# Performance work log

Measured on AMD Instinct MI355X. Metric: run time of the kernel, lower is better.

## Reference

```python
import jax, jax.numpy as jnp
import numpy as np

N, E, ENC, EMB, PI = 100000, 1600000, 128, 128, 98
ALPHA1, ALPHA2 = 0.5, 0.5


def setup_inputs() -> dict:
    key = jax.random.key(0)
    ks = jax.random.split(key, 20)
    s = 0.05
    return {
        "x": jax.random.normal(ks[0], (N, ENC), jnp.float32),
        "d2an": jax.random.normal(ks[1], (N, PI), jnp.float32),
        "ei0": jax.random.randint(ks[2], (2, E), 0, N, jnp.int32),
        "ew0": jax.random.uniform(ks[3], (E,), jnp.float32, 0.1, 4.0),
        "ei1": jax.random.randint(ks[4], (2, E), 0, N, jnp.int32),
        "ew1": jax.random.uniform(ks[5], (E,), jnp.float32, 0.1, 4.0),
        "nodeW1": jax.random.normal(ks[6], (ENC, ENC + PI), jnp.float32) * s,
        "nodeW2": jax.random.normal(ks[7], (ENC, ENC + PI), jnp.float32) * s,
        "W1a": jax.random.normal(ks[8], (EMB, ENC), jnp.float32) * s,
        "W1b": jax.random.normal(ks[9], (EMB, ENC), jnp.float32) * s,
        "W2a": jax.random.normal(ks[10], (EMB, ENC), jnp.float32) * s,
        "W2b": jax.random.normal(ks[11], (EMB, ENC), jnp.float32) * s,
        "W3a": jax.random.normal(ks[12], (EMB, EMB), jnp.float32) * s,
        "W3b": jax.random.normal(ks[13], (EMB, EMB), jnp.float32) * s,
        "W4a": jax.random.normal(ks[14], (EMB, EMB), jnp.float32) * s,
        "W4b": jax.random.normal(ks[15], (EMB, EMB), jnp.float32) * s,
    }


def _layer(x, ei, ew, W1, W2, nodeW, d2an, first):
    """PosKnnGNNLayer.forward: add self loops, optional nodeLin, GCN deg norm +
    edge norm, gather -> lin1/lin2 -> scale -> scatter-add (aggr='add')."""
    n = x.shape[0]
    loop = jnp.arange(n, dtype=ei.dtype)
    row = jnp.concatenate([ei[0], loop])          # source nodes (x_j)
    col = jnp.concatenate([ei[1], loop])          # target nodes (aggregation)
    attr = jnp.concatenate([ew, jnp.ones((n,), ew.dtype)])  # self-loop fill=1.0
    if first:
        x = jnp.concatenate([x, d2an], axis=1) @ nodeW.T
    deg = jax.ops.segment_sum(jnp.ones_like(attr), col, num_segments=n)
    dis = jnp.where(deg > 0, jax.lax.rsqrt(jnp.maximum(deg, 1.0)), 0.0)
    deg_norm = dis[row] * dis[col]                # [E']
    einv = attr ** -0.5
    einv = jnp.where(jnp.isinf(einv), 0.0, einv)
    einv = jnp.minimum(einv, 1.0)                 # clamp >1 to 1
    h1 = x @ W1.T                                 # [N, out]
    h2 = x @ W2.T
    msg = deg_norm[:, None] * h1[row] + einv[:, None] * h2[row]  # [E', out]
    return jax.ops.segment_sum(msg, col, num_segments=n)


def reference(x, d2an, ei0, ew0, ei1, ew1, nodeW1, nodeW2,
              W1a, W1b, W2a, W2b, W3a, W3b, W4a, W4b):
    # eval mode: dropout(p=0.3) is identity
    x0 = jax.nn.relu(_layer(x, ei0, ew0, W1a, W1b, nodeW1, d2an, True))
    x1 = jax.nn.relu(_layer(x, ei1, ew1, W2a, W2b, nodeW2, d2an, True))
    xm = ALPHA1 * x0 + ALPHA2 * x1
    x0 = jax.nn.relu(_layer(xm, ei0, ew0, W3a, W3b, None, None, False))
    x1 = jax.nn.relu(_layer(xm, ei1, ew1, W4a, W4b, None, None, False))
    return ALPHA1 * x0 + ALPHA2 * x1
```

## Files before the change

### kernel.cpp

```cpp
#include <hip/hip_runtime.h>
#include <hip/hip_fp16.h>
#include <stdint.h>

#define NN 100000
#define NE 1600000
#define ETOT (NE + NN)

typedef __attribute__((ext_vector_type(8))) short bf16x8;
typedef __attribute__((ext_vector_type(4))) float f32x4;
typedef __attribute__((ext_vector_type(4))) unsigned short us4;

__device__ __forceinline__ float bf2f(unsigned short u) {
    union { unsigned int i; float f; } x; x.i = ((unsigned int)u) << 16; return x.f;
}
__device__ __forceinline__ unsigned short f2bf(float f) {
    union { float f; unsigned int i; } x; x.f = f;
    unsigned int i = x.i;
    return (unsigned short)((i + 0x7FFFu + ((i >> 16) & 1u)) >> 16);
}
__device__ __forceinline__ int packab(float a, float b) {
    unsigned int ua = __half_as_ushort(__float2half_rn(a));
    unsigned int ub = __half_as_ushort(__float2half_rn(b));
    return (int)(ua | (ub << 16));
}
__device__ __forceinline__ float2 unpackab(int p) {
    float a = __half2float(__ushort_as_half((unsigned short)(p & 0xFFFF)));
    float b = __half2float(__ushort_as_half((unsigned short)(((unsigned int)p) >> 16)));
    return make_float2(a, b);
}

__global__ void k_init_deg(int* deg0, int* deg1) {
    int i = blockIdx.x * 256 + threadIdx.x;
    if (i < NN) { deg0[i] = 1; deg1[i] = 1; }
}

__global__ void k_count(const int* col0, const int* col1, int* deg0, int* deg1) {
    int t = blockIdx.x * 256 + threadIdx.x;
    if (t * 4 >= NE) return;
    const int* col = blockIdx.y ? col1 : col0;
    int* deg = blockIdx.y ? deg1 : deg0;
    int4 a = ((const int4*)col)[t];
    atomicAdd(&deg[a.x], 1); atomicAdd(&deg[a.y], 1);
    atomicAdd(&deg[a.z], 1); atomicAdd(&deg[a.w], 1);
}

__global__ void k_scan1(const int* deg0, const int* deg1, int* rp0, int* rp1s, int* bsum) {
    __shared__ int s[256];
    const int* deg = blockIdx.y ? deg1 : deg0;
    int* rp = (blockIdx.y ? rp1s : rp0) + 1;
    int* bs = bsum + blockIdx.y * 128;
    int tid = threadIdx.x;
    int base = blockIdx.x * 1024 + tid * 4;
    int v0 = 0, v1 = 0, v2 = 0, v3 = 0;
    if (base + 0 < NN) v0 = deg[base + 0];
    if (base + 1 < NN) v1 = deg[base + 1];
    if (base + 2 < NN) v2 = deg[base + 2];
    if (base + 3 < NN) v3 = deg[base + 3];
    int sum = v0 + v1 + v2 + v3;
    s[tid] = sum; __syncthreads();
    for (int off = 1; off < 256; off <<= 1) {
        int t = (tid >= off) ? s[tid - off] : 0;
        __syncthreads(); s[tid] += t; __syncthreads();
    }
    int run = s[tid] - sum;
    if (base + 0 < NN) { run += v0; rp[base + 0] = run; }
    if (base + 1 < NN) { run += v1; rp[base + 1] = run; }
    if (base + 2 < NN) { run += v2; rp[base + 2] = run; }
    if (base + 3 < NN) { run += v3; rp[base + 3] = run; }
    if (tid == 255) bs[blockIdx.x] = s[255];
}

__global__ void k_scan2(int* bsum, int nb) {
    __shared__ int s[128];
    int* bs = bsum + blockIdx.x * 128;
    int tid = threadIdx.x;
    int v = (tid < nb) ? bs[tid] : 0;
    s[tid] = v; __syncthreads();
    for (int off = 1; off < 128; off <<= 1) {
        int t = (tid >= off) ? s[tid - off] : 0;
        __syncthreads(); s[tid] += t; __syncthreads();
    }
    if (tid < nb) bs[tid] = s[tid] - v;
}

__global__ void k_scan3(int* rp0, int* rp1s, const int* bsum) {
    int* rowptr = blockIdx.y ? rp1s : rp0;
    int add = bsum[blockIdx.y * 128 + blockIdx.x];
    int tid = threadIdx.x;
    int base = blockIdx.x * 1024 + tid * 4;
    #pragma unroll
    for (int i = 0; i < 4; i++) {
        int idx = base + i;
        if (idx < NN) rowptr[idx + 1] += add;
    }
    if (blockIdx.x == 0 && tid == 0) rowptr[0] = 0;
}

__global__ void k_self(const int* rp0, const int* rp1s, const int* deg0, const int* deg1,
                       int2* eo0, int2* eo1, int* cur0, int* cur1, float* dis0, float* dis1) {
    int i = blockIdx.x * 256 + threadIdx.x;
    if (i >= NN) return;
    const int* rowptr = blockIdx.y ? rp1s : rp0;
    const int* deg = blockIdx.y ? deg1 : deg0;
    int2* eo = blockIdx.y ? eo1 : eo0;
    int* cursor = blockIdx.y ? cur1 : cur0;
    float* dis = blockIdx.y ? dis1 : dis0;
    int p = rowptr[i];
    float d = (float)deg[i];
    eo[p] = make_int2(i, packab(1.0f / d, 1.0f));
    cursor[i] = p + 1;
    dis[i] = rsqrtf(d);
}

__global__ void k_fill(const int* ei0, const float* ew0, const int* ei1, const float* ew1,
                       int* cur0, int* cur1, const float* dis0, const float* dis1,
                       int2* eo0, int2* eo1) {
    int slice = blockIdx.x & 7;
    int e = (blockIdx.x >> 3) * 256 + threadIdx.x;
    if (e >= NE) return;
    const int* er = blockIdx.y ? ei1 : ei0;
    int c = er[NE + e];
    int s = (int)((unsigned long long)(unsigned int)c * 8u / 100000u);
    if (s != slice) return;
    const float* ew = blockIdx.y ? ew1 : ew0;
    int* cursor = blockIdx.y ? cur1 : cur0;
    const float* dis = blockIdx.y ? dis1 : dis0;
    int2* eo = blockIdx.y ? eo1 : eo0;
    int r = er[e];
    float a = dis[r] * dis[c];
    float b = fminf(rsqrtf(ew[e]), 1.0f);
    int p = atomicAdd(&cursor[c], 1);
    eo[p] = make_int2(r, packab(a, b));
}

__global__ void k_packx(const float* x, const float* d2, unsigned short* Xc) {
    int idx = blockIdx.x * 256 + threadIdx.x;
    if (idx >= NN * 64) return;
    int r = idx >> 6, k4 = (idx & 63) << 2;
    us4 o;
    if (k4 < 128) {
        float4 v = *(const float4*)(x + (size_t)r * 128 + k4);
        o[0] = f2bf(v.x); o[1] = f2bf(v.y); o[2] = f2bf(v.z); o[3] = f2bf(v.w);
    } else {
        #pragma unroll
        for (int i = 0; i < 4; i++) {
            int k = k4 + i;
            float v = (k < 226) ? d2[(size_t)r * 98 + (k - 128)] : 0.f;
            o[i] = f2bf(v);
        }
    }
    *(us4*)(Xc + (size_t)r * 256 + k4) = o;
}

__global__ void k_packw(const float* wn1, const float* wn2,
                        const float* w1a, const float* w1b,
                        const float* w2a, const float* w2b,
                        const float* w3a, const float* w3b,
                        const float* w4a, const float* w4b,
                        unsigned short* Wfnode, unsigned short* WfL) {
    int idx = blockIdx.x * 256 + threadIdx.x;
    if (idx < 65536) {
        int j = idx & 7, lane = (idx >> 3) & 63, ct = (idx >> 9) & 15, ks = idx >> 13;
        int k = ks * 32 + (lane >> 4) * 8 + j;
        int c = ct * 16 + (lane & 15);
        float v = 0.f;
        if (k < 226) v = (c < 128) ? wn1[c * 226 + k] : wn2[(c - 128) * 226 + k];
        Wfnode[idx] = f2bf(v);
    } else if (idx < 196608) {
        int li = idx - 65536;
        int set = li >> 15, r = li & 32767;
        const float* wa = (set == 0) ? w1a : (set == 1) ? w2a : (set == 2) ? w3a : w4a;
        const float* wb = (set == 0) ? w1b : (set == 1) ? w2b : (set == 2) ? w3b : w4b;
        int j = r & 7, lane = (r >> 3) & 63, ct = (r >> 9) & 7, ks = r >> 12;
        int k = ks * 32 + (lane >> 4) * 8 + j;
        int c = ct * 16 + (lane & 15);
        float v = (k < 128) ? wa[c * 128 + k] : wb[c * 128 + (k - 128)];
        WfL[li] = f2bf(v);
    }
}

template <int SRST, int SOFF>
__global__ __launch_bounds__(256) void k_agg(const unsigned short* S,
                                             const int* rowptr, const int2* eg,
                                             unsigned short* G) {
    int c = blockIdx.x * 4 + (threadIdx.x >> 6);
    int lane = threadIdx.x & 63;
    if (c >= NN) return;
    float a0 = 0.f, a1 = 0.f, b0 = 0.f, b1 = 0.f;
    int jb = rowptr[c], je = rowptr[c + 1];
    const unsigned short* Sb = S + SOFF + lane * 2;
    int j = jb;
    for (; j + 16 <= je; j += 16) {
        int2 e[16]; unsigned int u[16];
        #pragma unroll
        for (int i = 0; i < 16; i++) e[i] = eg[j + i];
        #pragma unroll
        for (int i = 0; i < 16; i++)
            u[i] = *(const unsigned int*)(Sb + (size_t)e[i].x * SRST);
        #pragma unroll
        for (int i = 0; i < 16; i++) {
            float2 w = unpackab(e[i].y);
            float x0 = bf2f((unsigned short)(u[i] & 0xFFFF));
            float x1 = bf2f((unsigned short)(u[i] >> 16));
            a0 += w.x * x0; a1 += w.x * x1; b0 += w.y * x0; b1 += w.y * x1;
        }
    }
    for (; j + 4 <= je; j += 4) {
        int2 e[4]; unsigned int u[4];
        #pragma unroll
        for (int i = 0; i < 4; i++) e[i] = eg[j + i];
        #pragma unroll
        for (int i = 0; i < 4; i++)
            u[i] = *(const unsigned int*)(Sb + (size_t)e[i].x * SRST);
        #pragma unroll
        for (int i = 0; i < 4; i++) {
            float2 w = unpackab(e[i].y);
            float x0 = bf2f((unsigned short)(u[i] & 0xFFFF));
            float x1 = bf2f((unsigned short)(u[i] >> 16));
            a0 += w.x * x0; a1 += w.x * x1; b0 += w.y * x0; b1 += w.y * x1;
        }
    }
    for (; j < je; j++) {
        int2 e = eg[j];
        unsigned int u = *(const unsigned int*)(Sb + (size_t)e.x * SRST);
        float2 w = unpackab(e.y);
        float x0 = bf2f((unsigned short)(u & 0xFFFF));
        float x1 = bf2f((unsigned short)(u >> 16));
        a0 += w.x * x0; a1 += w.x * x1; b0 += w.y * x0; b1 += w.y * x1;
    }
    unsigned int* gd = (unsigned int*)(G + (size_t)c * 256);
    gd[lane]      = (unsigned int)f2bf(a0) | ((unsigned int)f2bf(a1) << 16);
    gd[64 + lane] = (unsigned int)f2bf(b0) | ((unsigned int)f2bf(b1) << 16);
}

template <int MODE>
__global__ __launch_bounds__(256) void k_gemm(const unsigned short* A, int arst,
                                              const unsigned short* Wf, int nct_total,
                                              unsigned short* outB, float* outF,
                                              const unsigned short* T, int orst) {
    int wave = threadIdx.x >> 6, lane = threadIdx.x & 63;
    int m = lane & 15, quad = lane >> 4;
    int row0 = blockIdx.x * 64 + wave * 16;
    int arow = row0 + m;
    bool rowok = arow < NN;
    const unsigned short* Ap = A + (size_t)arow * arst + quad * 8;
    int ctbase = blockIdx.y * 8;
    f32x4 acc[8];
    #pragma unroll
    for (int t = 0; t < 8; t++) acc[t] = (f32x4){0.f, 0.f, 0.f, 0.f};

    #pragma unroll
    for (int ks = 0; ks < 8; ks++) {
        bf16x8 a;
        if (rowok) a = *(const bf16x8*)(Ap + ks * 32);
        else       a = (bf16x8){0, 0, 0, 0, 0, 0, 0, 0};
        const unsigned short* wp = Wf + ((size_t)(ks * nct_total + ctbase) * 64 + lane) * 8;
        #pragma unroll
        for (int t = 0; t < 8; t++) {
            bf16x8 b = *(const bf16x8*)(wp + t * 512);
            acc[t] = __builtin_amdgcn_mfma_f32_16x16x32_bf16(a, b, acc[t], 0, 0, 0);
        }
    }

    int col0 = blockIdx.y * 128;
    #pragma unroll
    for (int t = 0; t < 8; t++) {
        int c = col0 + t * 16 + m;
        #pragma unroll
        for (int rg = 0; rg < 4; rg++) {
            int r = row0 + quad * 4 + rg;
            if (r < NN) {
                float v = acc[t][rg];
                if (MODE == 0) {
                    outB[(size_t)r * orst + c] = f2bf(v);
                } else {
                    float tv = bf2f(T[(size_t)r * 128 + c]);
                    float o = 0.5f * fmaxf(tv, 0.f) + 0.5f * fmaxf(v, 0.f);
                    if (MODE == 1) outB[(size_t)r * orst + c] = f2bf(o);
                    else           outF[(size_t)r * 128 + c] = o;
                }
            }
        }
    }
}

extern "C" void kernel_launch(void* const* d_in, const int* in_sizes, int n_in,
                              void* d_out, int out_size, void* d_ws, size_t ws_size,
                              hipStream_t stream) {
    const float* x      = (const float*)d_in[0];
    const float* d2an   = (const float*)d_in[1];
    const int*   ei0    = (const int*)d_in[2];
    const float* ew0    = (const float*)d_in[3];
    const int*   ei1    = (const int*)d_in[4];
    const float* ew1    = (const float*)d_in[5];
    const float* nodeW1 = (const float*)d_in[6];
    const float* nodeW2 = (const float*)d_in[7];
    const float* W1a = (const float*)d_in[8],  *W1b = (const float*)d_in[9];
    const float* W2a = (const float*)d_in[10], *W2b = (const float*)d_in[11];
    const float* W3a = (const float*)d_in[12], *W3b = (const float*)d_in[13];
    const float* W4a = (const float*)d_in[14], *W4b = (const float*)d_in[15];
    float* out = (float*)d_out;

    char* p = (char*)d_ws;
    auto alloc = [&](size_t bytes) -> char* {
        char* r = p; p += (bytes + 255) & ~(size_t)255; return r;
    };
    unsigned short* bufA   = (unsigned short*)alloc((size_t)NN * 256 * 2);
    unsigned short* bufB   = (unsigned short*)alloc((size_t)NN * 256 * 2);
    unsigned short* Tbuf   = (unsigned short*)alloc((size_t)NN * 128 * 2);
    unsigned short* Wfnode = (unsigned short*)alloc(65536 * 2);
    unsigned short* WfL    = (unsigned short*)alloc((size_t)4 * 32768 * 2);
    int*    deg0    = (int*)alloc((size_t)NN * 4);
    int*    deg1    = (int*)alloc((size_t)NN * 4);
    int*    rowptr0 = (int*)alloc((size_t)(NN + 1) * 4);
    int*    rowptr1 = (int*)alloc((size_t)(NN + 1) * 4);
    int*    cur0    = (int*)alloc((size_t)NN * 4);
    int*    cur1    = (int*)alloc((size_t)NN * 4);
    int*    bsum    = (int*)alloc(2 * 128 * 4);
    float*  dis0    = (float*)alloc((size_t)NN * 4);
    float*  dis1    = (float*)alloc((size_t)NN * 4);
    int2*   eo0     = (int2*)alloc((size_t)ETOT * 8);
    int2*   eo1     = (int2*)alloc((size_t)ETOT * 8);

    int nbN  = (NN + 255) / 256;
    int nbE1 = (NE + 255) / 256;
    int nbE4 = (NE / 4 + 255) / 256;
    int nbS  = (NN + 1023) / 1024;
    dim3 gP((NN + 63) / 64, 2);
    dim3 gL((NN + 63) / 64, 1);
    int nbA = (NN + 3) / 4;

    k_init_deg<<<nbN, 256, 0, stream>>>(deg0, deg1);
    k_count<<<dim3(nbE4, 2), 256, 0, stream>>>(ei0 + NE, ei1 + NE, deg0, deg1);
    k_scan1<<<dim3(nbS, 2), 256, 0, stream>>>(deg0, deg1, rowptr0, rowptr1, bsum);
    k_scan2<<<2, 128, 0, stream>>>(bsum, nbS);
    k_scan3<<<dim3(nbS, 2), 256, 0, stream>>>(rowptr0, rowptr1, bsum);
    k_self<<<dim3(nbN, 2), 256, 0, stream>>>(rowptr0, rowptr1, deg0, deg1,
                                             eo0, eo1, cur0, cur1, dis0, dis1);
    k_fill<<<dim3(nbE1 * 8, 2), 256, 0, stream>>>(ei0, ew0, ei1, ew1,
                                                  cur0, cur1, dis0, dis1, eo0, eo1);

    k_packx<<<(NN * 64 + 255) / 256, 256, 0, stream>>>(x, d2an, bufA);
    k_packw<<<768, 256, 0, stream>>>(nodeW1, nodeW2, W1a, W1b, W2a, W2b,
                                     W3a, W3b, W4a, W4b, Wfnode, WfL);

    k_gemm<0><<<gP, 256, 0, stream>>>(bufA, 256, Wfnode, 16, bufB, nullptr, nullptr, 256);
    k_agg<256, 0><<<nbA, 256, 0, stream>>>(bufB, rowptr0, eo0, bufA);
    k_gemm<0><<<gL, 256, 0, stream>>>(bufA, 256, WfL, 8, Tbuf, nullptr, nullptr, 128);
    k_agg<256, 128><<<nbA, 256, 0, stream>>>(bufB, rowptr1, eo1, bufA);
    k_gemm<1><<<gL, 256, 0, stream>>>(bufA, 256, WfL + 32768, 8, bufB, nullptr, Tbuf, 128);

    k_agg<128, 0><<<nbA, 256, 0, stream>>>(bufB, rowptr0, eo0, bufA);
    k_gemm<0><<<gL, 256, 0, stream>>>(bufA, 256, WfL + 2 * 32768, 8, Tbuf, nullptr, nullptr, 128);
    k_agg<128, 0><<<nbA, 256, 0, stream>>>(bufB, rowptr1, eo1, bufA);
    k_gemm<2><<<gL, 256, 0, stream>>>(bufA, 256, WfL + 3 * 32768, 8, nullptr, out, Tbuf, 128);
}
```

Baseline: 963.5 us.

## Replace atomic CSR fill with two-pass bucketed scatter using shared-memory counters

The single fill kernel re-read the destination array eight times, once per column slice, and claimed a slot per edge with a global atomic cursor. It is replaced by a bucketed counting sort. Per-block histograms over 512-node buckets are prefix-scanned into per-block base offsets, and edges are scattered into a staging buffer that reuses bufB, with the local column packed into the high bits of the row field. A final pass per bucket places records in CSR order using shared-memory atomics. This removes global atomics and the redundant reads, at the cost of three extra launches and an extra pass over the staging records.

```diff
diff --git a/kernel.cpp b/kernel.cpp
--- a/kernel.cpp
+++ b/kernel.cpp
@@ -5,6 +5,10 @@
 #define NN 100000
 #define NE 1600000
 #define ETOT (NE + NN)
+#define EPB 8192
+#define NBLK ((NE + EPB - 1) / EPB)
+#define NPB 512
+#define NBUK ((NN + NPB - 1) / NPB)
 
 typedef __attribute__((ext_vector_type(8))) short bf16x8;
 typedef __attribute__((ext_vector_type(4))) float f32x4;
@@ -97,40 +101,103 @@
 }
 
 __global__ void k_self(const int* rp0, const int* rp1s, const int* deg0, const int* deg1,
-                       int2* eo0, int2* eo1, int* cur0, int* cur1, float* dis0, float* dis1) {
+                       int2* eo0, int2* eo1, float* dis0, float* dis1) {
     int i = blockIdx.x * 256 + threadIdx.x;
     if (i >= NN) return;
     const int* rowptr = blockIdx.y ? rp1s : rp0;
     const int* deg = blockIdx.y ? deg1 : deg0;
     int2* eo = blockIdx.y ? eo1 : eo0;
-    int* cursor = blockIdx.y ? cur1 : cur0;
     float* dis = blockIdx.y ? dis1 : dis0;
     int p = rowptr[i];
     float d = (float)deg[i];
     eo[p] = make_int2(i, packab(1.0f / d, 1.0f));
-    cursor[i] = p + 1;
     dis[i] = rsqrtf(d);
 }
 
-__global__ void k_fill(const int* ei0, const float* ew0, const int* ei1, const float* ew1,
-                       int* cur0, int* cur1, const float* dis0, const float* dis1,
-                       int2* eo0, int2* eo1) {
-    int slice = blockIdx.x & 7;
-    int e = (blockIdx.x >> 3) * 256 + threadIdx.x;
-    if (e >= NE) return;
+__global__ __launch_bounds__(256) void k_cnt(const int* ei0, const int* ei1, int* cntm) {
+    __shared__ int h[NBUK];
+    const int* col = (blockIdx.y ? ei1 : ei0) + NE;
+    for (int i = threadIdx.x; i < NBUK; i += 256) h[i] = 0;
+    __syncthreads();
+    int base = blockIdx.x * EPB;
+    for (int i = 0; i < EPB / 256; i++) {
+        int e = base + i * 256 + threadIdx.x;
+        if (e < NE) atomicAdd(&h[col[e] >> 9], 1);
+    }
+    __syncthreads();
+    int* out = cntm + ((size_t)blockIdx.y * NBLK + blockIdx.x) * NBUK;
+    for (int i = threadIdx.x; i < NBUK; i += 256) out[i] = h[i];
+}
+
+__global__ __launch_bounds__(256) void k_base(const int* rp0, const int* rp1s,
+                                              const int* cntm, int* basem, int* btot) {
+    __shared__ int s[256];
+    int b = blockIdx.x;
+    const int* rowptr = blockIdx.y ? rp1s : rp0;
+    const int* cnt = cntm + (size_t)blockIdx.y * NBLK * NBUK;
+    int t = threadIdx.x;
+    int v = (t < NBLK) ? cnt[(size_t)t * NBUK + b] : 0;
+    s[t] = v; __syncthreads();
+    for (int off = 1; off < 256; off <<= 1) {
+        int u = (t >= off) ? s[t - off] : 0;
+        __syncthreads(); s[t] += u; __syncthreads();
+    }
+    int excl = s[t] - v;
+    int base0 = rowptr[b * NPB];
+    if (t < NBLK) basem[((size_t)blockIdx.y * NBLK + t) * NBUK + b] = base0 + excl;
+    if (t == 255) btot[blockIdx.y * NBUK + b] = s[255];
+}
+
+__global__ __launch_bounds__(256) void k_scat1(const int* ei0, const float* ew0,
+                                               const int* ei1, const float* ew1,
+                                               const float* dis0, const float* dis1,
+                                               const int* basem, int2* st0, int2* st1) {
+    __shared__ int lb[NBUK];
+    __shared__ int lc[NBUK];
     const int* er = blockIdx.y ? ei1 : ei0;
-    int c = er[NE + e];
-    int s = (int)((unsigned long long)(unsigned int)c * 8u / 100000u);
-    if (s != slice) return;
     const float* ew = blockIdx.y ? ew1 : ew0;
-    int* cursor = blockIdx.y ? cur1 : cur0;
     const float* dis = blockIdx.y ? dis1 : dis0;
+    int2* st = blockIdx.y ? st1 : st0;
+    const int* bm = basem + ((size_t)blockIdx.y * NBLK + blockIdx.x) * NBUK;
+    for (int i = threadIdx.x; i < NBUK; i += 256) { lb[i] = bm[i]; lc[i] = 0; }
+    __syncthreads();
+    int base = blockIdx.x * EPB;
+    for (int i = 0; i < EPB / 256; i++) {
+        int e = base + i * 256 + threadIdx.x;
+        if (e >= NE) break;
+        int r = er[e];
+        int c = er[NE + e];
+        int bkt = c >> 9;
+        int rank = atomicAdd(&lc[bkt], 1);
+        float a = dis[r] * dis[c];
+        float b = fminf(rsqrtf(ew[e]), 1.0f);
+        st[lb[bkt] + rank] = make_int2(r | ((c & 511) << 17), packab(a, b));
+    }
+}
+
+__global__ __launch_bounds__(256) void k_scat2(const int* rp0, const int* rp1s,
+                                               const int* btot,
+                                               const int2* st0, const int2* st1,
+                                               int2* eo0, int2* eo1) {
+    __shared__ int lcur[NPB];
+    int b = blockIdx.x;
+    const int* rowptr = blockIdx.y ? rp1s : rp0;
+    const int2* st = blockIdx.y ? st1 : st0;
     int2* eo = blockIdx.y ? eo1 : eo0;
-    int r = er[e];
-    float a = dis[r] * dis[c];
-    float b = fminf(rsqrtf(ew[e]), 1.0f);
-    int p = atomicAdd(&cursor[c], 1);
-    eo[p] = make_int2(r, packab(a, b));
+    int nstart = b * NPB;
+    for (int i = threadIdx.x; i < NPB; i += 256) {
+        int node = nstart + i;
+        if (node < NN) lcur[i] = rowptr[node] + 1;
+    }
+    __syncthreads();
+    int s0 = rowptr[nstart];
+    int tot = btot[blockIdx.y * NBUK + b];
+    for (int j = s0 + (int)threadIdx.x; j < s0 + tot; j += 256) {
+        int2 rec = st[j];
+        int cl = (rec.x >> 17) & 511;
+        int pos = atomicAdd(&lcur[cl], 1);
+        eo[pos] = make_int2(rec.x & 0x1FFFF, rec.y);
+    }
 }
 
 __global__ void k_packx(const float* x, const float* d2, unsigned short* Xc) {
@@ -314,16 +381,19 @@
     int*    deg1    = (int*)alloc((size_t)NN * 4);
     int*    rowptr0 = (int*)alloc((size_t)(NN + 1) * 4);
     int*    rowptr1 = (int*)alloc((size_t)(NN + 1) * 4);
-    int*    cur0    = (int*)alloc((size_t)NN * 4);
-    int*    cur1    = (int*)alloc((size_t)NN * 4);
     int*    bsum    = (int*)alloc(2 * 128 * 4);
     float*  dis0    = (float*)alloc((size_t)NN * 4);
     float*  dis1    = (float*)alloc((size_t)NN * 4);
     int2*   eo0     = (int2*)alloc((size_t)ETOT * 8);
     int2*   eo1     = (int2*)alloc((size_t)ETOT * 8);
+    int*    cntm    = (int*)alloc((size_t)2 * NBLK * NBUK * 4);
+    int*    basem   = (int*)alloc((size_t)2 * NBLK * NBUK * 4);
+    int*    btot    = (int*)alloc((size_t)2 * NBUK * 4);
+
+    int2* st0 = (int2*)bufB;
+    int2* st1 = st0 + ETOT;
 
     int nbN  = (NN + 255) / 256;
-    int nbE1 = (NE + 255) / 256;
     int nbE4 = (NE / 4 + 255) / 256;
     int nbS  = (NN + 1023) / 1024;
     dim3 gP((NN + 63) / 64, 2);
@@ -336,9 +406,13 @@
     k_scan2<<<2, 128, 0, stream>>>(bsum, nbS);
     k_scan3<<<dim3(nbS, 2), 256, 0, stream>>>(rowptr0, rowptr1, bsum);
     k_self<<<dim3(nbN, 2), 256, 0, stream>>>(rowptr0, rowptr1, deg0, deg1,
-                                             eo0, eo1, cur0, cur1, dis0, dis1);
-    k_fill<<<dim3(nbE1 * 8, 2), 256, 0, stream>>>(ei0, ew0, ei1, ew1,
-                                                  cur0, cur1, dis0, dis1, eo0, eo1);
+                                             eo0, eo1, dis0, dis1);
+    k_cnt<<<dim3(NBLK, 2), 256, 0, stream>>>(ei0, ei1, cntm);
+    k_base<<<dim3(NBUK, 2), 256, 0, stream>>>(rowptr0, rowptr1, cntm, basem, btot);
+    k_scat1<<<dim3(NBLK, 2), 256, 0, stream>>>(ei0, ew0, ei1, ew1,
+                                               dis0, dis1, basem, st0, st1);
+    k_scat2<<<dim3(NBUK, 2), 256, 0, stream>>>(rowptr0, rowptr1, btot,
+                                               st0, st1, eo0, eo1);
 
     k_packx<<<(NN * 64 + 255) / 256, 256, 0, stream>>>(x, d2an, bufA);
     k_packw<<<768, 256, 0, stream>>>(nodeW1, nodeW2, W1a, W1b, W2a, W2b,
```

New measurement: 916.4 us. 4.9% less time.
